# Performance work log

Hardware: AMD Instinct MI355X
Metric: run time of the kernel (lower is better)

## Reference

```python
import jax, jax.numpy as jnp
import numpy as np

B, T, D = 2, 2048, 2048
H, G = 16, 4            # query heads, kv groups
HD = D // H             # head_dim = 128
GS = H // G             # group_size = 4
EPS = 1e-6
ROPE_BASE = 10000.0


def setup_inputs() -> dict:
    key = jax.random.key(0)
    ks = jax.random.split(key, 5)
    s = 0.02
    return {
        "x": jax.random.normal(ks[0], (B, T, D), jnp.float32),
        "Wq": jax.random.normal(ks[1], (H * HD, D), jnp.float32) * s,
        "Wk": jax.random.normal(ks[2], (G * HD, D), jnp.float32) * s,
        "Wv": jax.random.normal(ks[3], (G * HD, D), jnp.float32) * s,
        "Wo": jax.random.normal(ks[4], (D, H * HD), jnp.float32) * s,
        "qn_w": jnp.ones((HD,), jnp.float32),
        "kn_w": jnp.ones((HD,), jnp.float32),
    }


def _rmsnorm(x, w):
    var = jnp.mean(x * x, axis=-1, keepdims=True)
    return x * jax.lax.rsqrt(var + EPS) * w


def _rope_tables(t, d):
    inv_freq = 1.0 / (ROPE_BASE ** (jnp.arange(0, d, 2, dtype=jnp.float32) / d))
    freqs = jnp.arange(t, dtype=jnp.float32)[:, None] * inv_freq[None, :]
    emb = jnp.concatenate([freqs, freqs], axis=-1)  # [T, d]
    return jnp.cos(emb), jnp.sin(emb)


def _apply_rope(x, cos, sin):
    # x: [b, h, t, d]
    d2 = x.shape[-1] // 2
    x1, x2 = x[..., :d2], x[..., d2:]
    rot = jnp.concatenate([-x2, x1], axis=-1)
    return x * cos + rot * sin


def reference(x, Wq, Wk, Wv, Wo, qn_w, kn_w):
    b, t, _ = x.shape
    q = (x @ Wq.T).reshape(b, t, H, HD).transpose(0, 2, 1, 3)  # [b,H,t,hd]
    k = (x @ Wk.T).reshape(b, t, G, HD).transpose(0, 2, 1, 3)  # [b,G,t,hd]
    v = (x @ Wv.T).reshape(b, t, G, HD).transpose(0, 2, 1, 3)

    q = _rmsnorm(q, qn_w)
    k = _rmsnorm(k, kn_w)

    cos, sin = _rope_tables(t, HD)
    q = _apply_rope(q, cos, sin)
    k = _apply_rope(k, cos, sin)

    # torch code scales q by hd^-0.5, then SDPA applies default hd^-0.5 again
    scale = (HD ** -0.5) * (HD ** -0.5)

    # GQA without materializing repeat_interleave: group query heads
    qg = q.reshape(b, G, GS, t, HD)
    scores = jnp.einsum("bgxqd,bgkd->bgxqk", qg, k) * scale  # [b,G,GS,t,t]
    causal = jnp.tril(jnp.ones((t, t), bool))
    scores = jnp.where(causal, scores, -jnp.inf)
    attn = jax.nn.softmax(scores, axis=-1)
    ctx = jnp.einsum("bgxqk,bgkd->bgxqd", attn, v)  # [b,G,GS,t,hd]
    ctx = ctx.reshape(b, H, t, HD).transpose(0, 2, 1, 3).reshape(b, t, H * HD)
    return ctx @ Wo.T
```

## Files before the change

kernel.cpp:

```cpp
#include <hip/hip_runtime.h>
#include <hip/hip_bf16.h>

#define B_ 2
#define T_ 2048
#define D_ 2048
#define H_ 16
#define G_ 4
#define HD_ 128
#define GS_ (H_/G_)

typedef _Float16 half8 __attribute__((ext_vector_type(8)));
typedef _Float16 half2_t __attribute__((ext_vector_type(2)));
typedef float f32x4 __attribute__((ext_vector_type(4)));
typedef float f32x16 __attribute__((ext_vector_type(16)));
typedef int int4_t __attribute__((ext_vector_type(4)));

#define KV_TILE_BYTES 36864
#define KROW_F16 136
#define VROW_F16 72
#define VBASE_F16 8704

#define C0_ 1048576
#define C1_ 1572864
#define C2_ 1703936
#define C3_ 1835008
#define C4_ 2359296
__global__ void cvt_rope(const float* __restrict__ sx, const float* __restrict__ sq,
                         const float* __restrict__ sk, const float* __restrict__ sv,
                         const float* __restrict__ so,
                         _Float16* __restrict__ dx, _Float16* __restrict__ dq,
                         _Float16* __restrict__ dk, _Float16* __restrict__ dv,
                         _Float16* __restrict__ dw,
                         float* __restrict__ cosT, float* __restrict__ sinT) {
    int blk = blockIdx.x, tid = threadIdx.x;
    if (blk < 2048) {
        int g = blk * 256 + tid;
        for (; g < C4_; g += 2048 * 256) {
            const float* src; _Float16* dst; int local;
            if (g < C0_)      { src = sx; dst = dx; local = g; }
            else if (g < C1_) { src = sq; dst = dq; local = g - C0_; }
            else if (g < C2_) { src = sk; dst = dk; local = g - C1_; }
            else if (g < C3_) { src = sv; dst = dv; local = g - C2_; }
            else              { src = so; dst = dw; local = g - C3_; }
            f32x4 a = *((const f32x4*)src + local * 2);
            f32x4 b = *((const f32x4*)src + local * 2 + 1);
            half8 hv;
            hv[0] = (_Float16)a[0]; hv[1] = (_Float16)a[1];
            hv[2] = (_Float16)a[2]; hv[3] = (_Float16)a[3];
            hv[4] = (_Float16)b[0]; hv[5] = (_Float16)b[1];
            hv[6] = (_Float16)b[2]; hv[7] = (_Float16)b[3];
            *((half8*)dst + local) = hv;
        }
    } else {
        int i = (blk - 2048) * 256 + tid;
        int t = i >> 6, l = i & 63;
        float inv_freq = powf(10000.0f, -((float)(2 * l)) / 128.0f);
        float a = (float)t * inv_freq;
        cosT[i] = cosf(a);
        sinT[i] = sinf(a);
    }
}

__global__ void __launch_bounds__(256) gemm_tile(const _Float16* __restrict__ A,
                                                 const _Float16* __restrict__ B0,
                                                 float* __restrict__ C0, int n0t,
                                                 const _Float16* __restrict__ B1,
                                                 float* __restrict__ C1, int n1t,
                                                 const _Float16* __restrict__ B2,
                                                 float* __restrict__ C2, int n2t,
                                                 int Kd) {
    __shared__ _Float16 sA[2][128 * 32];
    __shared__ _Float16 sB[2][128 * 32];

    int tid = threadIdx.x;
    int w = tid >> 6, lane = tid & 63;
    int l15 = lane & 15, g4 = lane >> 4;
    int wm = w >> 1, wn = w & 1;

    int y = blockIdx.y;
    const _Float16* Bsel;
    float* Csel;
    int ldc, cb;
    if (y < n0t)            { Bsel = B0; Csel = C0; ldc = n0t * 128; cb = y; }
    else if (y < n0t + n1t) { Bsel = B1; Csel = C1; ldc = n1t * 128; cb = y - n0t; }
    else                    { Bsel = B2; Csel = C2; ldc = n2t * 128; cb = y - n0t - n1t; }

    const _Float16* Ab = A + (size_t)(blockIdx.x * 128) * Kd;
    const _Float16* Bb = Bsel + (size_t)(cb * 128) * Kd;

    int s0 = w * 128 + lane;
    int s1 = s0 + 64;
    size_t ga0 = (size_t)(s0 >> 2) * Kd + (s0 & 3) * 8;
    size_t ga1 = (size_t)(s1 >> 2) * Kd + (s1 & 3) * 8;

    #define STAGE(BUF, K0)                                                                     \
        do {                                                                                   \
            _Float16* a0_ = &sA[BUF][0] + (size_t)(w * 2) * 512;                               \
            _Float16* a1_ = &sA[BUF][0] + (size_t)(w * 2 + 1) * 512;                           \
            _Float16* b0_ = &sB[BUF][0] + (size_t)(w * 2) * 512;                               \
            _Float16* b1_ = &sB[BUF][0] + (size_t)(w * 2 + 1) * 512;                           \
            __builtin_amdgcn_global_load_lds(                                                  \
                (const __attribute__((address_space(1))) unsigned int*)(Ab + ga0 + (K0)),      \
                (__attribute__((address_space(3))) unsigned int*)a0_, 16, 0, 0);               \
            __builtin_amdgcn_global_load_lds(                                                  \
                (const __attribute__((address_space(1))) unsigned int*)(Ab + ga1 + (K0)),      \
                (__attribute__((address_space(3))) unsigned int*)a1_, 16, 0, 0);               \
            __builtin_amdgcn_global_load_lds(                                                  \
                (const __attribute__((address_space(1))) unsigned int*)(Bb + ga0 + (K0)),      \
                (__attribute__((address_space(3))) unsigned int*)b0_, 16, 0, 0);               \
            __builtin_amdgcn_global_load_lds(                                                  \
                (const __attribute__((address_space(1))) unsigned int*)(Bb + ga1 + (K0)),      \
                (__attribute__((address_space(3))) unsigned int*)b1_, 16, 0, 0);               \
        } while (0)

    f32x4 acc[4][4];
    #pragma unroll
    for (int i = 0; i < 4; i++)
        #pragma unroll
        for (int j = 0; j < 4; j++) acc[i][j] = (f32x4){0.f, 0.f, 0.f, 0.f};

    int nIt = Kd >> 5;
    STAGE(0, 0);
    if (nIt > 1) STAGE(1, 32);

    for (int it = 0; it < nIt; ++it) {
        int cur = it & 1;
        if (it + 1 < nIt) asm volatile("s_waitcnt vmcnt(4)" ::: "memory");
        else              asm volatile("s_waitcnt vmcnt(0)" ::: "memory");
        __builtin_amdgcn_sched_barrier(0);
        __builtin_amdgcn_s_barrier();
        __builtin_amdgcn_sched_barrier(0);

        half8 af[4], bf[4];
        #pragma unroll
        for (int mi = 0; mi < 4; mi++)
            af[mi] = *(const half8*)&sA[cur][(wm * 64 + mi * 16 + l15) * 32 + g4 * 8];
        #pragma unroll
        for (int ni = 0; ni < 4; ni++)
            bf[ni] = *(const half8*)&sB[cur][(wn * 64 + ni * 16 + l15) * 32 + g4 * 8];

        #pragma unroll
        for (int mi = 0; mi < 4; mi++)
            #pragma unroll
            for (int ni = 0; ni < 4; ni++)
                acc[mi][ni] = __builtin_amdgcn_mfma_f32_16x16x32_f16(af[mi], bf[ni], acc[mi][ni], 0, 0, 0);

        __builtin_amdgcn_sched_barrier(0);
        asm volatile("" ::: "memory");
        __builtin_amdgcn_s_barrier();
        __builtin_amdgcn_sched_barrier(0);
        if (it + 2 < nIt) STAGE(cur, (size_t)(it + 2) * 32);
    }
    #undef STAGE

    int rbase = blockIdx.x * 128 + wm * 64 + g4 * 4;
    int cbase = cb * 128 + wn * 64 + l15;
    #pragma unroll
    for (int mi = 0; mi < 4; mi++)
        #pragma unroll
        for (int r = 0; r < 4; r++) {
            float* crow = Csel + (size_t)(rbase + mi * 16 + r) * ldc + cbase;
            #pragma unroll
            for (int ni = 0; ni < 4; ni++) crow[ni * 16] = acc[mi][ni][r];
        }
}

__global__ void __launch_bounds__(256) norm_pack(const float* __restrict__ Qf,
                                                 const float* __restrict__ Kf,
                                                 const float* __restrict__ vf,
                                                 const float* __restrict__ qw,
                                                 const float* __restrict__ kw,
                                                 const float* __restrict__ cosT,
                                                 const float* __restrict__ sinT,
                                                 _Float16* __restrict__ qH,
                                                 _Float16* __restrict__ img) {
    int blk = blockIdx.x, tid = threadIdx.x;
    if (blk < 20480) {
        int gw = (blk * 256 + tid) >> 6;
        int lane = tid & 63;
        bool isQ = gw < (B_ * T_ * H_);
        int row_i = isQ ? gw : gw - (B_ * T_ * H_);
        int heads = isQ ? H_ : G_;
        const float* wv = isQ ? qw : kw;
        const float* row = (isQ ? Qf : Kf) + (size_t)row_i * HD_;
        int t = (row_i / heads) % T_;
        float x0 = row[lane];
        float x1 = row[lane + 64];
        float ss = x0 * x0 + x1 * x1;
        #pragma unroll
        for (int off = 1; off < 64; off <<= 1) ss += __shfl_xor(ss, off);
        float inv = rsqrtf(ss * (1.0f / 128.0f) + 1e-6f);
        float n0 = x0 * inv * wv[lane];
        float n1 = x1 * inv * wv[lane + 64];
        float c = cosT[t * 64 + lane];
        float s = sinT[t * 64 + lane];
        float r0 = n0 * c - n1 * s;
        float r1 = n1 * c + n0 * s;
        if (isQ) {
            qH[(size_t)row_i * HD_ + lane]      = (_Float16)(r0 * (1.0f / 128.0f));
            qH[(size_t)row_i * HD_ + lane + 64] = (_Float16)(r1 * (1.0f / 128.0f));
        } else {
            int b = row_i / (T_ * G_);
            int rem = row_i - b * (T_ * G_);
            int g = rem - (rem / G_) * G_;
            int bid = (b * 4 + g) * 32 + (t >> 6);
            _Float16* kout = img + (size_t)bid * (KV_TILE_BYTES / 2) + (t & 63) * KROW_F16;
            kout[lane]      = (_Float16)r0;
            kout[lane + 64] = (_Float16)r1;
        }
    } else {
        int vb = blk - 20480;
        int tile = vb & 31, g = (vb >> 5) & 3, b = vb >> 7;
        _Float16* out = img + (size_t)vb * (KV_TILE_BYTES / 2);
        #pragma unroll
        for (int it = 0; it < 5; it++) {
            int vi = tid + 256 * it;
            if (vi < 128 * 9) {
                int d = vi / 9, gr = vi % 9;
                half8 hv = (half8){0, 0, 0, 0, 0, 0, 0, 0};
                if (gr < 8) {
                    const float* src = vf + ((size_t)((b * T_ + tile * 64 + gr * 8) * G_ + g)) * HD_ + d;
                    #pragma unroll
                    for (int j = 0; j < 8; j++) hv[j] = (_Float16)src[(size_t)j * (G_ * HD_)];
                }
                *(half8*)(out + VBASE_F16 + (size_t)vi * 8) = hv;
            }
        }
    }
}

__global__ void __launch_bounds__(256, 2) attn_mfma5(const _Float16* __restrict__ qh,
                                                     const _Float16* __restrict__ kvimg,
                                                     _Float16* __restrict__ ctx) {
    int id = blockIdx.x;
    int hlf = id >> 8, rr0 = id & 255;
    int qb = hlf ? (15 - (rr0 & 15)) : (rr0 & 15);
    int hb = (rr0 >> 4) | (hlf << 4);
    int h = hb & 15, b = hb >> 4;
    int g = h >> 2;

    int tid = threadIdx.x;
    int w = tid >> 6, lane = tid & 63;
    int l31 = lane & 31, hi = lane >> 5;

    __shared__ __align__(16) char sKV[2][KV_TILE_BYTES];

    int qW = qb * 128 + w * 32;
    int qme = qW + l31;

    half8 qfrag[8];
    {
        const _Float16* qrow = qh + ((size_t)(b * T_ + qme)) * (H_ * HD_) + h * HD_ + hi * 8;
        #pragma unroll
        for (int ks = 0; ks < 8; ks++) qfrag[ks] = *(const half8*)(qrow + ks * 16);
    }

    f32x16 o[4];
    #pragma unroll
    for (int dt2 = 0; dt2 < 4; dt2++)
        #pragma unroll
        for (int r = 0; r < 16; r++) o[dt2][r] = 0.f;
    float m = -INFINITY, lsum = 0.f;

    const char* ibase = (const char*)kvimg + (size_t)((b * 4 + g) * 32) * KV_TILE_BYTES;

    #define STAGE_T(BUF, KT)                                                                       \
        do {                                                                                       \
            const char* src_ = ibase + (size_t)(KT) * KV_TILE_BYTES;                               \
            char* dst_ = &sKV[BUF][0];                                                             \
            _Pragma("unroll")                                                                      \
            for (int i_ = 0; i_ < 9; i_++) {                                                       \
                int c_ = w + 4 * i_;                                                               \
                __builtin_amdgcn_global_load_lds(                                                  \
                    (const __attribute__((address_space(1))) unsigned int*)(src_ + c_ * 1024 + lane * 16), \
                    (__attribute__((address_space(3))) unsigned int*)(dst_ + c_ * 1024 + lane * 16), 16, 0, 0); \
            }                                                                                      \
        } while (0)

    int nt = 2 * qb + 2;
    int ktmax_w = (qW + 31) >> 6;

    STAGE_T(0, 0);
    STAGE_T(1, 1);

    for (int kt = 0; kt < nt; kt++) {
        int cur = kt & 1;
        if (kt + 1 < nt) asm volatile("s_waitcnt vmcnt(9)" ::: "memory");
        else             asm volatile("s_waitcnt vmcnt(0)" ::: "memory");
        __builtin_amdgcn_sched_barrier(0);
        __builtin_amdgcn_s_barrier();
        __builtin_amdgcn_sched_barrier(0);

        if (kt <= ktmax_w) {
            const char* bufK = &sKV[cur][0];
            const char* bufV = &sKV[cur][0] + VBASE_F16 * 2;

            f32x16 stc[2];
            #pragma unroll
            for (int kt2 = 0; kt2 < 2; kt2++)
                #pragma unroll
                for (int r = 0; r < 16; r++) stc[kt2][r] = 0.f;

            __builtin_amdgcn_s_setprio(1);
            #pragma unroll
            for (int ks = 0; ks < 8; ks++) {
                #pragma unroll
                for (int kt2 = 0; kt2 < 2; kt2++) {
                    half8 kfr = *(const half8*)(bufK + (kt2 * 32 + l31) * (KROW_F16 * 2) + ks * 32 + hi * 16);
                    stc[kt2] = __builtin_amdgcn_mfma_f32_32x32x16_f16(kfr, qfrag[ks], stc[kt2], 0, 0, 0);
                }
            }
            __builtin_amdgcn_s_setprio(0);

            #pragma unroll
            for (int kt2 = 0; kt2 < 2; kt2++)
                #pragma unroll
                for (int reg = 0; reg < 16; reg++) {
                    int key = kt * 64 + kt2 * 32 + 8 * (reg >> 2) + 4 * hi + (reg & 3);
                    float v = stc[kt2][reg];
                    stc[kt2][reg] = (key <= qme) ? v : -INFINITY;
                }

            float pmax = -INFINITY;
            #pragma unroll
            for (int kt2 = 0; kt2 < 2; kt2++)
                #pragma unroll
                for (int reg = 0; reg < 16; reg++) pmax = fmaxf(pmax, stc[kt2][reg]);
            pmax = fmaxf(pmax, __shfl_xor(pmax, 32));

            if (__any(!(pmax - m <= 8.0f))) {
                float nm = fmaxf(m, pmax);
                float alpha = __expf(m - nm);
                lsum *= alpha;
                #pragma unroll
                for (int reg = 0; reg < 16; reg++) {
                    float ar = __shfl(alpha, 8 * (reg >> 2) + 4 * hi + (reg & 3));
                    #pragma unroll
                    for (int dt2 = 0; dt2 < 4; dt2++) o[dt2][reg] *= ar;
                }
                m = nm;
            }

            float rsum = 0.f;
            #pragma unroll
            for (int kt2 = 0; kt2 < 2; kt2++)
                #pragma unroll
                for (int reg = 0; reg < 16; reg++) {
                    float e = __expf(stc[kt2][reg] - m);
                    stc[kt2][reg] = e;
                    rsum += e;
                }
            rsum += __shfl_xor(rsum, 32);
            lsum += rsum;

            int pk[16];
            #pragma unroll
            for (int kt2 = 0; kt2 < 2; kt2++)
                #pragma unroll
                for (int oo = 0; oo < 4; oo++)
                    #pragma unroll
                    for (int c = 0; c < 2; c++) {
                        half2_t hp;
                        hp[0] = (_Float16)stc[kt2][4 * oo + 2 * c];
                        hp[1] = (_Float16)stc[kt2][4 * oo + 2 * c + 1];
                        pk[kt2 * 8 + 2 * oo + c] = __builtin_bit_cast(int, hp);
                    }

            __builtin_amdgcn_s_setprio(1);
            #pragma unroll
            for (int ks = 0; ks < 4; ks++) {
                int base = (ks >> 1) * 8 + (ks & 1) * 4;
                int z0 = hi ? pk[base + 0] : pk[base + 2];
                int z1 = hi ? pk[base + 1] : pk[base + 3];
                int xz0 = __shfl_xor(z0, 32);
                int xz1 = __shfl_xor(z1, 32);
                int4_t pi;
                pi[0] = hi ? xz0 : pk[base + 0];
                pi[1] = hi ? xz1 : pk[base + 1];
                pi[2] = hi ? pk[base + 2] : xz0;
                pi[3] = hi ? pk[base + 3] : xz1;
                half8 pfrag = __builtin_bit_cast(half8, pi);
                #pragma unroll
                for (int dt2 = 0; dt2 < 4; dt2++) {
                    half8 vfr = *(const half8*)(bufV + (dt2 * 32 + l31) * (VROW_F16 * 2) + ks * 32 + hi * 16);
                    o[dt2] = __builtin_amdgcn_mfma_f32_32x32x16_f16(pfrag, vfr, o[dt2], 0, 0, 0);
                }
            }
            __builtin_amdgcn_s_setprio(0);
        }

        __builtin_amdgcn_sched_barrier(0);
        asm volatile("" ::: "memory");
        __builtin_amdgcn_s_barrier();
        __builtin_amdgcn_sched_barrier(0);
        if (kt + 2 < nt) STAGE_T(cur, kt + 2);
    }
    #undef STAGE_T

    float invl = 1.0f / lsum;
    #pragma unroll
    for (int reg = 0; reg < 16; reg++) {
        int qrow = 8 * (reg >> 2) + 4 * hi + (reg & 3);
        float ir = __shfl(invl, qrow);
        _Float16* orow = ctx + (size_t)(b * T_ + qW + qrow) * (H_ * HD_) + h * HD_ + l31;
        #pragma unroll
        for (int dt2 = 0; dt2 < 4; dt2++)
            orow[dt2 * 32] = (_Float16)(o[dt2][reg] * ir);
    }
}

extern "C" void kernel_launch(void* const* d_in, const int* in_sizes, int n_in,
                              void* d_out, int out_size, void* d_ws, size_t ws_size,
                              hipStream_t stream) {
    const float* x   = (const float*)d_in[0];
    const float* Wq  = (const float*)d_in[1];
    const float* Wk  = (const float*)d_in[2];
    const float* Wv  = (const float*)d_in[3];
    const float* Wo  = (const float*)d_in[4];
    const float* qnw = (const float*)d_in[5];
    const float* knw = (const float*)d_in[6];
    float* out = (float*)d_out;

    char* ws = (char*)d_ws;
    size_t off = 0;
    auto alloc = [&](size_t bytes) {
        char* p = ws + off;
        off += (bytes + 255) & ~(size_t)255;
        return p;
    };
    _Float16* x_h  = (_Float16*)alloc((size_t)B_ * T_ * D_ * 2);
    _Float16* wq_h = (_Float16*)alloc((size_t)H_ * HD_ * D_ * 2);
    _Float16* wk_h = (_Float16*)alloc((size_t)G_ * HD_ * D_ * 2);
    _Float16* wv_h = (_Float16*)alloc((size_t)G_ * HD_ * D_ * 2);
    _Float16* wo_h = (_Float16*)alloc((size_t)D_ * H_ * HD_ * 2);
    float* q_f = (float*)alloc((size_t)B_ * T_ * H_ * HD_ * 4);
    float* k_f = (float*)alloc((size_t)B_ * T_ * G_ * HD_ * 4);
    float* v_f = (float*)alloc((size_t)B_ * T_ * G_ * HD_ * 4);
    _Float16* ctx_h = (_Float16*)alloc((size_t)B_ * T_ * H_ * HD_ * 2);
    float* cosT = (float*)alloc((size_t)T_ * 64 * 4);
    float* sinT = (float*)alloc((size_t)T_ * 64 * 4);

    _Float16* q_h   = x_h;
    _Float16* kvimg = wq_h;

    cvt_rope<<<2560, 256, 0, stream>>>(x, Wq, Wk, Wv, Wo, x_h, wq_h, wk_h, wv_h, wo_h,
                                       cosT, sinT);

    gemm_tile<<<dim3(32, 24), 256, 0, stream>>>(x_h, wq_h, q_f, 16,
                                                wk_h, k_f, 4,
                                                wv_h, v_f, 4, D_);

    norm_pack<<<20736, 256, 0, stream>>>(q_f, k_f, v_f, qnw, knw, cosT, sinT, q_h, kvimg);

    attn_mfma5<<<512, 256, 0, stream>>>(q_h, kvimg, ctx_h);

    gemm_tile<<<dim3(32, 16), 256, 0, stream>>>(ctx_h, wo_h, out, 16,
                                                nullptr, nullptr, 0,
                                                nullptr, nullptr, 0, H_ * HD_);
}
```

Measured before the change: 214.2 us.

## Fuse Q/K RMSNorm and RoPE into the projection GEMM epilogue

The QKV projection GEMM now applies per-head RMSNorm, RoPE and the fp16 packing for Q and K directly in its epilogue, staging each 64-row half of the accumulator tile through shared memory. This removes the fp32 round trip of Q and K through global memory and the large norm_pack launch. V still goes to fp32 and is packed by a smaller standalone kernel. The q_h and kvimg buffers now get their own workspace instead of aliasing x_h and wq_h, which the fused GEMM still reads while writing them. The epilogue adds shared-memory staging, two block barriers and scattered writes to the GEMM.

```diff
diff --git a/kernel.cpp b/kernel.cpp
--- a/kernel.cpp
+++ b/kernel.cpp
@@ -68,7 +68,13 @@
                                                  float* __restrict__ C1, int n1t,
                                                  const _Float16* __restrict__ B2,
                                                  float* __restrict__ C2, int n2t,
-                                                 int Kd) {
+                                                 int Kd, int fuse,
+                                                 const float* __restrict__ qw,
+                                                 const float* __restrict__ kw,
+                                                 const float* __restrict__ cosT,
+                                                 const float* __restrict__ sinT,
+                                                 _Float16* __restrict__ qH,
+                                                 _Float16* __restrict__ img) {
     __shared__ _Float16 sA[2][128 * 32];
     __shared__ _Float16 sB[2][128 * 32];
 
@@ -153,78 +159,87 @@
     }
     #undef STAGE
 
-    int rbase = blockIdx.x * 128 + wm * 64 + g4 * 4;
-    int cbase = cb * 128 + wn * 64 + l15;
+    if (!fuse || y >= n0t + n1t) {
+        int rbase = blockIdx.x * 128 + wm * 64 + g4 * 4;
+        int cbase = cb * 128 + wn * 64 + l15;
+        #pragma unroll
+        for (int mi = 0; mi < 4; mi++)
+            #pragma unroll
+            for (int r = 0; r < 4; r++) {
+                float* crow = Csel + (size_t)(rbase + mi * 16 + r) * ldc + cbase;
+                #pragma unroll
+                for (int ni = 0; ni < 4; ni++) crow[ni * 16] = acc[mi][ni][r];
+            }
+        return;
+    }
+
+    bool isQ = (y < n0t);
+    const float* wv = isQ ? qw : kw;
+    float* sC = (float*)&sA[0][0];
+
     #pragma unroll
-    for (int mi = 0; mi < 4; mi++)
-        #pragma unroll
-        for (int r = 0; r < 4; r++) {
-            float* crow = Csel + (size_t)(rbase + mi * 16 + r) * ldc + cbase;
-            #pragma unroll
-            for (int ni = 0; ni < 4; ni++) crow[ni * 16] = acc[mi][ni][r];
+    for (int ch = 0; ch < 2; ch++) {
+        __syncthreads();
+        if (wm == ch) {
+            #pragma unroll
+            for (int mi = 0; mi < 4; mi++)
+                #pragma unroll
+                for (int ni = 0; ni < 4; ni++)
+                    #pragma unroll
+                    for (int r = 0; r < 4; r++)
+                        sC[(mi * 16 + g4 * 4 + r) * 128 + wn * 64 + ni * 16 + l15] = acc[mi][ni][r];
         }
+        __syncthreads();
+        #pragma unroll
+        for (int i = 0; i < 16; i++) {
+            int rloc = w * 16 + i;
+            int grow = blockIdx.x * 128 + ch * 64 + rloc;
+            int t = grow & (T_ - 1);
+            float x0 = sC[rloc * 128 + lane];
+            float x1 = sC[rloc * 128 + lane + 64];
+            float ss = x0 * x0 + x1 * x1;
+            #pragma unroll
+            for (int off = 1; off < 64; off <<= 1) ss += __shfl_xor(ss, off);
+            float inv = rsqrtf(ss * (1.0f / 128.0f) + 1e-6f);
+            float n0 = x0 * inv * wv[lane];
+            float n1 = x1 * inv * wv[lane + 64];
+            float c = cosT[t * 64 + lane];
+            float s = sinT[t * 64 + lane];
+            float r0 = n0 * c - n1 * s;
+            float r1 = n1 * c + n0 * s;
+            if (isQ) {
+                _Float16* qrow = qH + (size_t)grow * (H_ * HD_) + cb * HD_;
+                qrow[lane]      = (_Float16)(r0 * (1.0f / 128.0f));
+                qrow[lane + 64] = (_Float16)(r1 * (1.0f / 128.0f));
+            } else {
+                int b = grow >> 11;
+                int bid = (b * 4 + cb) * 32 + (t >> 6);
+                _Float16* kout = img + (size_t)bid * (KV_TILE_BYTES / 2) + (t & 63) * KROW_F16;
+                kout[lane]      = (_Float16)r0;
+                kout[lane + 64] = (_Float16)r1;
+            }
+        }
+    }
 }
 
-__global__ void __launch_bounds__(256) norm_pack(const float* __restrict__ Qf,
-                                                 const float* __restrict__ Kf,
-                                                 const float* __restrict__ vf,
-                                                 const float* __restrict__ qw,
-                                                 const float* __restrict__ kw,
-                                                 const float* __restrict__ cosT,
-                                                 const float* __restrict__ sinT,
-                                                 _Float16* __restrict__ qH,
-                                                 _Float16* __restrict__ img) {
-    int blk = blockIdx.x, tid = threadIdx.x;
-    if (blk < 20480) {
-        int gw = (blk * 256 + tid) >> 6;
-        int lane = tid & 63;
-        bool isQ = gw < (B_ * T_ * H_);
-        int row_i = isQ ? gw : gw - (B_ * T_ * H_);
-        int heads = isQ ? H_ : G_;
-        const float* wv = isQ ? qw : kw;
-        const float* row = (isQ ? Qf : Kf) + (size_t)row_i * HD_;
-        int t = (row_i / heads) % T_;
-        float x0 = row[lane];
-        float x1 = row[lane + 64];
-        float ss = x0 * x0 + x1 * x1;
-        #pragma unroll
-        for (int off = 1; off < 64; off <<= 1) ss += __shfl_xor(ss, off);
-        float inv = rsqrtf(ss * (1.0f / 128.0f) + 1e-6f);
-        float n0 = x0 * inv * wv[lane];
-        float n1 = x1 * inv * wv[lane + 64];
-        float c = cosT[t * 64 + lane];
-        float s = sinT[t * 64 + lane];
-        float r0 = n0 * c - n1 * s;
-        float r1 = n1 * c + n0 * s;
-        if (isQ) {
-            qH[(size_t)row_i * HD_ + lane]      = (_Float16)(r0 * (1.0f / 128.0f));
-            qH[(size_t)row_i * HD_ + lane + 64] = (_Float16)(r1 * (1.0f / 128.0f));
-        } else {
-            int b = row_i / (T_ * G_);
-            int rem = row_i - b * (T_ * G_);
-            int g = rem - (rem / G_) * G_;
-            int bid = (b * 4 + g) * 32 + (t >> 6);
-            _Float16* kout = img + (size_t)bid * (KV_TILE_BYTES / 2) + (t & 63) * KROW_F16;
-            kout[lane]      = (_Float16)r0;
-            kout[lane + 64] = (_Float16)r1;
-        }
-    } else {
-        int vb = blk - 20480;
-        int tile = vb & 31, g = (vb >> 5) & 3, b = vb >> 7;
-        _Float16* out = img + (size_t)vb * (KV_TILE_BYTES / 2);
-        #pragma unroll
-        for (int it = 0; it < 5; it++) {
-            int vi = tid + 256 * it;
-            if (vi < 128 * 9) {
-                int d = vi / 9, gr = vi % 9;
-                half8 hv = (half8){0, 0, 0, 0, 0, 0, 0, 0};
-                if (gr < 8) {
-                    const float* src = vf + ((size_t)((b * T_ + tile * 64 + gr * 8) * G_ + g)) * HD_ + d;
-                    #pragma unroll
-                    for (int j = 0; j < 8; j++) hv[j] = (_Float16)src[(size_t)j * (G_ * HD_)];
-                }
-                *(half8*)(out + VBASE_F16 + (size_t)vi * 8) = hv;
-            }
+__global__ void __launch_bounds__(256) pack_v(const float* __restrict__ vf,
+                                              _Float16* __restrict__ img) {
+    int vb = blockIdx.x;
+    int tile = vb & 31, g = (vb >> 5) & 3, b = vb >> 7;
+    int tid = threadIdx.x;
+    _Float16* out = img + (size_t)vb * (KV_TILE_BYTES / 2);
+    #pragma unroll
+    for (int it = 0; it < 5; it++) {
+        int vi = tid + 256 * it;
+        if (vi < 128 * 9) {
+            int d = vi / 9, gr = vi % 9;
+            half8 hv = (half8){0, 0, 0, 0, 0, 0, 0, 0};
+            if (gr < 8) {
+                const float* src = vf + ((size_t)((b * T_ + tile * 64 + gr * 8) * G_ + g)) * HD_ + d;
+                #pragma unroll
+                for (int j = 0; j < 8; j++) hv[j] = (_Float16)src[(size_t)j * (G_ * HD_)];
+            }
+            *(half8*)(out + VBASE_F16 + (size_t)vi * 8) = hv;
         }
     }
 }
@@ -433,28 +448,28 @@
     _Float16* wk_h = (_Float16*)alloc((size_t)G_ * HD_ * D_ * 2);
     _Float16* wv_h = (_Float16*)alloc((size_t)G_ * HD_ * D_ * 2);
     _Float16* wo_h = (_Float16*)alloc((size_t)D_ * H_ * HD_ * 2);
-    float* q_f = (float*)alloc((size_t)B_ * T_ * H_ * HD_ * 4);
-    float* k_f = (float*)alloc((size_t)B_ * T_ * G_ * HD_ * 4);
     float* v_f = (float*)alloc((size_t)B_ * T_ * G_ * HD_ * 4);
     _Float16* ctx_h = (_Float16*)alloc((size_t)B_ * T_ * H_ * HD_ * 2);
     float* cosT = (float*)alloc((size_t)T_ * 64 * 4);
     float* sinT = (float*)alloc((size_t)T_ * 64 * 4);
-
-    _Float16* q_h   = x_h;
-    _Float16* kvimg = wq_h;
+    _Float16* q_h = (_Float16*)alloc((size_t)B_ * T_ * H_ * HD_ * 2);
+    _Float16* kvimg = (_Float16*)alloc((size_t)256 * KV_TILE_BYTES);
 
     cvt_rope<<<2560, 256, 0, stream>>>(x, Wq, Wk, Wv, Wo, x_h, wq_h, wk_h, wv_h, wo_h,
                                        cosT, sinT);
 
-    gemm_tile<<<dim3(32, 24), 256, 0, stream>>>(x_h, wq_h, q_f, 16,
-                                                wk_h, k_f, 4,
-                                                wv_h, v_f, 4, D_);
-
-    norm_pack<<<20736, 256, 0, stream>>>(q_f, k_f, v_f, qnw, knw, cosT, sinT, q_h, kvimg);
+    gemm_tile<<<dim3(32, 24), 256, 0, stream>>>(x_h, wq_h, nullptr, 16,
+                                                wk_h, nullptr, 4,
+                                                wv_h, v_f, 4, D_, 1,
+                                                qnw, knw, cosT, sinT, q_h, kvimg);
+
+    pack_v<<<256, 256, 0, stream>>>(v_f, kvimg);
 
     attn_mfma5<<<512, 256, 0, stream>>>(q_h, kvimg, ctx_h);
 
     gemm_tile<<<dim3(32, 16), 256, 0, stream>>>(ctx_h, wo_h, out, 16,
                                                 nullptr, nullptr, 0,
-                                                nullptr, nullptr, 0, H_ * HD_);
+                                                nullptr, nullptr, 0, H_ * HD_, 0,
+                                                nullptr, nullptr, nullptr, nullptr,
+                                                nullptr, nullptr);
 }
```

After: 208.0 us. 2.9% less time.
